# Kernel tuning notes

Hardware: AMD Instinct MI355X
Metric: run time of the kernel (lower is better)

## Reference

```python
import jax, jax.numpy as jnp
import numpy as np

IN_FEATURES = 64
WIDTH = 64
GRID_POINTS = 64   # num control points / basis functions
DEGREE = 3
BATCH = 32768
LN_EPS = 1e-5


def make_knots():
    # clamped knot vector on [0, 1]: length = GRID_POINTS + DEGREE + 1
    knot_count = GRID_POINTS + DEGREE + 1
    knots = np.zeros(knot_count, dtype=np.float32)
    knots[-(DEGREE + 1):] = 1.0
    interior = knot_count - 2 * (DEGREE + 1)
    if interior > 0:
        knots[DEGREE + 1: DEGREE + 1 + interior] = np.linspace(0.0, 1.0, interior + 2, dtype=np.float32)[1:-1]
    return jnp.asarray(knots)


def bspline_basis(x, knots):
    # x: [B, F] in (0,1); vectorized Cox-de Boor across batch and features
    xx = x[..., None]                      # [B, F, 1]
    left, right = knots[:-1], knots[1:]
    b = ((xx >= left) & (xx < right)).astype(x.dtype)      # [B, F, n_basis]
    last = ((x >= left[-1]) & (x <= right[-1])).astype(x.dtype)
    b = jnp.concatenate([b[..., :-1], last[..., None]], axis=-1)
    n_basis = knots.shape[0] - 1
    for d in range(1, DEGREE + 1):
        upper = n_basis - d
        i = np.arange(upper)
        k_i, k_id = knots[i], knots[i + d]
        k_i1, k_id1 = knots[i + 1], knots[i + d + 1]
        den1, den2 = k_id - k_i, k_id1 - k_i1
        w1 = jnp.where(den1 > 0, (xx - k_i) / jnp.where(den1 > 0, den1, 1.0), 0.0)
        w2 = jnp.where(den2 > 0, (k_id1 - xx) / jnp.where(den2 > 0, den2, 1.0), 0.0)
        b = w1 * b[..., :upper] + w2 * b[..., 1:upper + 1]
    return b  # [B, F, GRID_POINTS]


def setup_inputs() -> dict:
    key = jax.random.key(0)
    ks = jax.random.split(key, 6)
    coeff_init = float(np.sqrt(2.0 / (GRID_POINTS * IN_FEATURES)))
    return {
        "inputs": jax.random.normal(ks[0], (BATCH, IN_FEATURES), dtype=jnp.float32),
        "input_shift": 0.1 * jax.random.normal(ks[1], (IN_FEATURES,), dtype=jnp.float32),
        "input_log_scale": 0.1 * jax.random.normal(ks[2], (IN_FEATURES,), dtype=jnp.float32),
        "spline_coeffs": coeff_init * jax.random.normal(ks[3], (IN_FEATURES, GRID_POINTS, WIDTH), dtype=jnp.float32),
        "skip_W": jax.random.normal(ks[4], (WIDTH, IN_FEATURES), dtype=jnp.float32) / np.sqrt(IN_FEATURES),
        "skip_b": 0.01 * jax.random.normal(ks[5], (WIDTH,), dtype=jnp.float32),
        "bias": jnp.zeros((WIDTH,), dtype=jnp.float32),
        "ln_gamma": jnp.ones((WIDTH,), dtype=jnp.float32),
        "ln_beta": jnp.zeros((WIDTH,), dtype=jnp.float32),
        "knots": make_knots(),
    }


def reference(inputs, input_shift, input_log_scale, spline_coeffs, skip_W, skip_b, bias, ln_gamma, ln_beta, knots):
    scale = jax.nn.softplus(input_log_scale) + 0.001
    normalised = jax.nn.sigmoid((inputs - input_shift) * scale)     # [B, F]
    basis = bspline_basis(normalised, knots)                        # [B, F, G]
    spline_mix = jnp.einsum('bfg,fgw->bw', basis, spline_coeffs)    # [B, W]
    skip = inputs @ skip_W.T + skip_b
    c = spline_mix + skip + bias
    mean = jnp.mean(c, axis=-1, keepdims=True)
    var = jnp.mean((c - mean) ** 2, axis=-1, keepdims=True)
    y = (c - mean) / jnp.sqrt(var + LN_EPS) * ln_gamma + ln_beta
    return jax.nn.gelu(y, approximate=False)
```

## Files before the change

### kernel.cpp

```cpp
#include <hip/hip_runtime.h>
#include <math.h>


#define NTHREADS 512
#define ROWSB 32
#define SLABF 16384

typedef short bf16x8 __attribute__((ext_vector_type(8)));
typedef float f32x4  __attribute__((ext_vector_type(4)));

#if __has_builtin(__builtin_amdgcn_sdot4)
#define SDOT4(a, b, c) __builtin_amdgcn_sdot4((int)(a), (int)(b), (c), false)
#else
__device__ __forceinline__ int sdot4_sw(unsigned a, unsigned b, int c) {
    return c + (int)(signed char)(a) * (int)(signed char)(b)
             + (int)(signed char)(a >> 8)  * (int)(signed char)(b >> 8)
             + (int)(signed char)(a >> 16) * (int)(signed char)(b >> 16)
             + (int)(signed char)(a >> 24) * (int)(signed char)(b >> 24);
}
#define SDOT4(a, b, c) sdot4_sw((a), (b), (c))
#endif

__device__ __forceinline__ unsigned int f2bf1(float f) {
    unsigned int u = __float_as_uint(f);
    return (u + 0x7fffu + ((u >> 16) & 1u)) >> 16;
}
__device__ __forceinline__ unsigned int q8(float v) {
    const float s = fminf(fmaxf(v * 512.f, -127.f), 127.f);
    return (unsigned int)((int)rintf(s)) & 255u;
}

__global__ __launch_bounds__(256) void kan_prep(
    const float* __restrict__ coeff_g,
    unsigned char* __restrict__ ws8)
{
    const int idx = blockIdx.x * 256 + threadIdx.x;
    const int f = idx / 3904;
    const int rem = idx - f * 3904;
    const int g0 = rem >> 6, w = rem & 63;
    const float* src = coeff_g + ((size_t)f << 12) + (g0 << 6) + w;
    const unsigned int d = q8(src[0])
                         | (q8(src[64])  << 8)
                         | (q8(src[128]) << 16)
                         | (q8(src[192]) << 24);
    *(unsigned int*)(ws8 + ((size_t)f << 14) + (g0 << 8) + (w << 2)) = d;
}

#define DOT4Q(WP, AV) do { \
    doti[0] = SDOT4((WP), (AV).x, doti[0]); \
    doti[1] = SDOT4((WP), (AV).y, doti[1]); \
    doti[2] = SDOT4((WP), (AV).z, doti[2]); \
    doti[3] = SDOT4((WP), (AV).w, doti[3]); } while (0)

template<bool PRE>
__global__ __launch_bounds__(NTHREADS, 6) void kan_fused(
    const float* __restrict__ x_g,
    const float* __restrict__ shift_g,
    const float* __restrict__ lsc_g,
    const float* __restrict__ coeff_g,
    const float* __restrict__ skipW_g,
    const float* __restrict__ skipb_g,
    const float* __restrict__ bias_g,
    const float* __restrict__ gamma_g,
    const float* __restrict__ beta_g,
    const float* __restrict__ knots_g,
    const unsigned char* __restrict__ ws8,
    float* __restrict__ out_g)
{
    __shared__ float  xin[64][ROWSB];
    __shared__ unsigned short xb[32 * 64];
    __shared__ unsigned short wst[64 * 64];
    __shared__ float  skps[32][64];
    __shared__ uint2  wtabd[2][32][20];
    __shared__ float  knot_s[68];
    __shared__ float  scale_s[64];
    __shared__ float  shift_s[64];

    const int t = threadIdx.x;
    const int row0 = blockIdx.x * ROWSB;

    auto basis_group = [&](int gb) {
        const int fc_ = t >> 5, r_ = t & 31;
        const int feat = (gb << 4) + fc_;
        const float xs = (xin[feat][r_] - shift_s[feat]) * scale_s[feat];
        const float xq = 1.f / (1.f + __expf(-xs));
        int m = (int)floorf(xq * 61.f);
        m = m < 0 ? 0 : (m > 60 ? 60 : m);
        const float u = fmaf(xq, 61.f, -(float)m);
        float N0, N1, N2, N3;
        if (__builtin_expect(m >= 2 && m <= 58, 1)) {
            const float omu = 1.f - u;
            const float u2 = u * u, u3 = u2 * u;
            N0 = omu * omu * omu * (1.f / 6.f);
            N3 = u3 * (1.f / 6.f);
            N1 = 0.5f * u3 - u2 + (2.f / 3.f);
            N2 = 1.f - N0 - N1 - N3;
        } else {
            const int i = m + 3;
            float left[4], right[4], N[4];
            N[0] = 1.f;
            #pragma unroll
            for (int j = 1; j <= 3; ++j) {
                left[j]  = xq - knot_s[i + 1 - j];
                right[j] = knot_s[i + j] - xq;
                float saved = 0.f;
                #pragma unroll
                for (int rr = 0; rr < j; ++rr) {
                    const float temp = N[rr] * __builtin_amdgcn_rcpf(right[rr + 1] + left[j - rr]);
                    N[rr] = saved + right[rr + 1] * temp;
                    saved = left[j - rr] * temp;
                }
                N[j] = saved;
            }
            N0 = N[0]; N1 = N[1]; N2 = N[2]; N3 = N[3];
        }
        const unsigned int q0 = (unsigned int)(int)(fmaxf(N0, 0.f) * 126.f + 0.5f);
        const unsigned int q1 = (unsigned int)(int)(fmaxf(N1, 0.f) * 126.f + 0.5f);
        const unsigned int q2 = (unsigned int)(int)(fmaxf(N2, 0.f) * 126.f + 0.5f);
        const unsigned int q3 = (unsigned int)(int)(fmaxf(N3, 0.f) * 126.f + 0.5f);
        wtabd[gb & 1][r_][fc_] = make_uint2(q0 | (q1 << 8) | (q2 << 16) | (q3 << 24),
                                            (unsigned int)(m << 8));
    };

    {
        const int r = t >> 4, f0 = (t & 15) << 2;
        const float4 a = *((const float4*)(x_g + (size_t)(row0 + r) * 64 + f0));
        xin[f0 + 0][r] = a.x; xin[f0 + 1][r] = a.y;
        xin[f0 + 2][r] = a.z; xin[f0 + 3][r] = a.w;
        uint2 p;
        p.x = f2bf1(a.x) | (f2bf1(a.y) << 16);
        p.y = f2bf1(a.z) | (f2bf1(a.w) << 16);
        const int byte = r * 128 + ((((t & 15) << 3)) ^ ((r & 7) << 4));
        *(uint2*)((char*)xb + byte) = p;
    }
    {
        const int w = t >> 3, f0 = (t & 7) << 3;
        const float4* src = (const float4*)(skipW_g + (size_t)w * 64 + f0);
        const float4 a0 = src[0], a1 = src[1];
        uint4 p;
        p.x = f2bf1(a0.x) | (f2bf1(a0.y) << 16);
        p.y = f2bf1(a0.z) | (f2bf1(a0.w) << 16);
        p.z = f2bf1(a1.x) | (f2bf1(a1.y) << 16);
        p.w = f2bf1(a1.z) | (f2bf1(a1.w) << 16);
        const int byte = w * 128 + ((((t & 7) << 4)) ^ ((w & 7) << 4));
        *(uint4*)((char*)wst + byte) = p;
    }
    if (t < 64) {
        scale_s[t] = log1pf(__expf(lsc_g[t])) + 0.001f;
        shift_s[t] = shift_g[t];
    }
    if (t < 68) knot_s[t] = knots_g[t];
    __syncthreads();

    const int lane = t & 63;
    const int wave = t >> 6;

    {
        const int mtile = wave >> 2;
        const int ntile = wave & 3;
        const int arow = mtile * 16 + (lane & 15);
        const int bcol = ntile * 16 + (lane & 15);
        const int koff = (lane >> 4) << 4;
        f32x4 acc = {0.f, 0.f, 0.f, 0.f};
        #pragma unroll
        for (int kb = 0; kb < 2; ++kb) {
            const int kbyte = (kb << 6) + koff;
            const bf16x8 af = *(const bf16x8*)((const char*)xb
                                + arow * 128 + (kbyte ^ ((arow & 7) << 4)));
            const bf16x8 bfr = *(const bf16x8*)((const char*)wst
                                + bcol * 128 + (kbyte ^ ((bcol & 7) << 4)));
            acc = __builtin_amdgcn_mfma_f32_16x16x32_bf16(af, bfr, acc, 0, 0, 0);
        }
        #pragma unroll
        for (int rr = 0; rr < 4; ++rr)
            skps[mtile * 16 + ((lane >> 4) << 2) + rr][bcol] = acc[rr];
    }

    const int wc   = lane & 15;
    const int rsub = lane >> 4;
    const int row  = (wave << 2) + rsub;
    const int w4   = wc << 2;
    const int wcb  = wc << 4;

    int doti[4] = {0, 0, 0, 0};
    float facc[4] = {0.f, 0.f, 0.f, 0.f};

    basis_group(0);
    __syncthreads();

    for (int g = 0; g < 4; ++g) {
        const uint2* wrow = &wtabd[g & 1][row][0];
        if (PRE) {
            const unsigned char* const gbase = ws8 + ((size_t)g << 18);
            const uint4 wpa = *(const uint4*)(wrow + 0);
            const uint4 wpb = *(const uint4*)(wrow + 2);
            const uint4 wpc = *(const uint4*)(wrow + 4);
            const uint4 wpd = *(const uint4*)(wrow + 6);
            const uint4 A0 = *(const uint4*)(gbase + (0 << 14) + (wpa.y | wcb));
            const uint4 A1 = *(const uint4*)(gbase + (1 << 14) + (wpa.w | wcb));
            const uint4 A2 = *(const uint4*)(gbase + (2 << 14) + (wpb.y | wcb));
            const uint4 A3 = *(const uint4*)(gbase + (3 << 14) + (wpb.w | wcb));
            const uint4 A4 = *(const uint4*)(gbase + (4 << 14) + (wpc.y | wcb));
            const uint4 A5 = *(const uint4*)(gbase + (5 << 14) + (wpc.w | wcb));
            const uint4 A6 = *(const uint4*)(gbase + (6 << 14) + (wpd.y | wcb));
            const uint4 A7 = *(const uint4*)(gbase + (7 << 14) + (wpd.w | wcb));
            if (g < 3) basis_group(g + 1);
            DOT4Q(wpa.x, A0); DOT4Q(wpa.z, A1);
            DOT4Q(wpb.x, A2); DOT4Q(wpb.z, A3);
            DOT4Q(wpc.x, A4); DOT4Q(wpc.z, A5);
            DOT4Q(wpd.x, A6); DOT4Q(wpd.z, A7);
            const uint4 wpe = *(const uint4*)(wrow + 8);
            const uint4 wpf = *(const uint4*)(wrow + 10);
            const uint4 wpg = *(const uint4*)(wrow + 12);
            const uint4 wph = *(const uint4*)(wrow + 14);
            const uint4 B0 = *(const uint4*)(gbase + (8 << 14)  + (wpe.y | wcb));
            const uint4 B1 = *(const uint4*)(gbase + (9 << 14)  + (wpe.w | wcb));
            const uint4 B2 = *(const uint4*)(gbase + (10 << 14) + (wpf.y | wcb));
            const uint4 B3 = *(const uint4*)(gbase + (11 << 14) + (wpf.w | wcb));
            const uint4 B4 = *(const uint4*)(gbase + (12 << 14) + (wpg.y | wcb));
            const uint4 B5 = *(const uint4*)(gbase + (13 << 14) + (wpg.w | wcb));
            const uint4 B6 = *(const uint4*)(gbase + (14 << 14) + (wph.y | wcb));
            const uint4 B7 = *(const uint4*)(gbase + (15 << 14) + (wph.w | wcb));
            DOT4Q(wpe.x, B0); DOT4Q(wpe.z, B1);
            DOT4Q(wpf.x, B2); DOT4Q(wpf.z, B3);
            DOT4Q(wpg.x, B4); DOT4Q(wpg.z, B5);
            DOT4Q(wph.x, B6); DOT4Q(wph.z, B7);
        } else {
            if (g < 3) basis_group(g + 1);
            #pragma unroll 2
            for (int fc = 0; fc < 16; ++fc) {
                const int f = (g << 4) + fc;
                const uint2 wv = wrow[fc];
                const float* cb = coeff_g + ((size_t)f << 12) + (wv.y >> 2) + w4;
                const float4 c0 = *((const float4*)cb);
                const float4 c1 = *((const float4*)(cb + 64));
                const float4 c2 = *((const float4*)(cb + 128));
                const float4 c3 = *((const float4*)(cb + 192));
                const float q0 = (float)(wv.x & 255u);
                const float q1 = (float)((wv.x >> 8) & 255u);
                const float q2 = (float)((wv.x >> 16) & 255u);
                const float q3 = (float)((wv.x >> 24) & 255u);
                facc[0] += q0 * c0.x + q1 * c1.x + q2 * c2.x + q3 * c3.x;
                facc[1] += q0 * c0.y + q1 * c1.y + q2 * c2.y + q3 * c3.y;
                facc[2] += q0 * c0.z + q1 * c1.z + q2 * c2.z + q3 * c3.z;
                facc[3] += q0 * c0.w + q1 * c1.w + q2 * c2.w + q3 * c3.w;
            }
        }
        __syncthreads();
    }

    const float4 sk = *((const float4*)(&skps[row][w4]));
    const float4 sb = *((const float4*)(skipb_g + w4));
    const float4 bi = *((const float4*)(bias_g + w4));
    const float4 ga = *((const float4*)(gamma_g + w4));
    const float4 be = *((const float4*)(beta_g + w4));
    const float add_[4] = {sk.x + sb.x + bi.x, sk.y + sb.y + bi.y,
                           sk.z + sb.z + bi.z, sk.w + sb.w + bi.w};
    const float gam[4] = {ga.x, ga.y, ga.z, ga.w};
    const float bet[4] = {be.x, be.y, be.z, be.w};
    const float cs = PRE ? (1.f / (512.f * 126.f)) : (1.f / 126.f);

    float c[4];
    #pragma unroll
    for (int k = 0; k < 4; ++k) {
        const float sp = PRE ? (float)doti[k] * cs : facc[k] * cs;
        c[k] = sp + add_[k];
    }
    float s = c[0] + c[1] + c[2] + c[3];
    s += __shfl_xor(s, 1); s += __shfl_xor(s, 2);
    s += __shfl_xor(s, 4); s += __shfl_xor(s, 8);
    const float mean = s * 0.015625f;
    float v = 0.f;
    #pragma unroll
    for (int k = 0; k < 4; ++k) { const float d = c[k] - mean; v += d * d; }
    v += __shfl_xor(v, 1); v += __shfl_xor(v, 2);
    v += __shfl_xor(v, 4); v += __shfl_xor(v, 8);
    const float inv = rsqrtf(v * 0.015625f + 1e-5f);
    float o[4];
    #pragma unroll
    for (int k = 0; k < 4; ++k) {
        const float y = (c[k] - mean) * inv * gam[k] + bet[k];
        o[k] = 0.5f * y * (1.f + erff(y * 0.70710678118f));
    }
    *((float4*)(out_g + (size_t)(row0 + row) * 64 + w4)) =
        make_float4(o[0], o[1], o[2], o[3]);
}

extern "C" void kernel_launch(void* const* d_in, const int* in_sizes, int n_in,
                              void* d_out, int out_size, void* d_ws, size_t ws_size,
                              hipStream_t stream) {
    (void)in_sizes; (void)n_in; (void)out_size;
    const bool pre = (ws_size >= (size_t)(64 * SLABF));
    if (pre) {
        kan_prep<<<976, 256, 0, stream>>>((const float*)d_in[3], (unsigned char*)d_ws);
        kan_fused<true><<<1024, NTHREADS, 0, stream>>>(
            (const float*)d_in[0], (const float*)d_in[1], (const float*)d_in[2],
            (const float*)d_in[3], (const float*)d_in[4], (const float*)d_in[5],
            (const float*)d_in[6], (const float*)d_in[7], (const float*)d_in[8],
            (const float*)d_in[9], (const unsigned char*)d_ws, (float*)d_out);
    } else {
        kan_fused<false><<<1024, NTHREADS, 0, stream>>>(
            (const float*)d_in[0], (const float*)d_in[1], (const float*)d_in[2],
            (const float*)d_in[3], (const float*)d_in[4], (const float*)d_in[5],
            (const float*)d_in[6], (const float*)d_in[7], (const float*)d_in[8],
            (const float*)d_in[9], (const unsigned char*)d_ws, (float*)d_out);
    }
}
```

Before: 35.41 us.

## Compute all basis weights upfront and run a single sync-free gather loop

Replaces the four-stage double-buffered basis/gather pipeline with one pass in which each thread computes basis weights for four features of a row. It writes them into a padded per-row table that aliases the shared-memory area already used by the skip-GEMM operands. The main loop then walks all 64 features with no per-group barriers. Launch bounds rise to 8 blocks per CU, and the aliasing shrinks LDS use to make room. The trade is the loss of overlap between basis computation and gather loads, and tighter register limits.

New measurement: 32.65 us. -7.8%, faster.

```diff
diff --git a/kernel.cpp b/kernel.cpp
--- a/kernel.cpp
+++ b/kernel.cpp
@@ -5,6 +5,7 @@
 #define NTHREADS 512
 #define ROWSB 32
 #define SLABF 16384
+#define WTROW 544
 
 typedef short bf16x8 __attribute__((ext_vector_type(8)));
 typedef float f32x4  __attribute__((ext_vector_type(4)));
@@ -53,7 +54,7 @@
     doti[3] = SDOT4((WP), (AV).w, doti[3]); } while (0)
 
 template<bool PRE>
-__global__ __launch_bounds__(NTHREADS, 6) void kan_fused(
+__global__ __launch_bounds__(NTHREADS, 8) void kan_fused(
     const float* __restrict__ x_g,
     const float* __restrict__ shift_g,
     const float* __restrict__ lsc_g,
@@ -67,60 +68,17 @@
     const unsigned char* __restrict__ ws8,
     float* __restrict__ out_g)
 {
-    __shared__ float  xin[64][ROWSB];
-    __shared__ unsigned short xb[32 * 64];
-    __shared__ unsigned short wst[64 * 64];
-    __shared__ float  skps[32][64];
-    __shared__ uint2  wtabd[2][32][20];
-    __shared__ float  knot_s[68];
-    __shared__ float  scale_s[64];
-    __shared__ float  shift_s[64];
+    __shared__ float xin[64][ROWSB];
+    __shared__ char  uA[32 * WTROW] __attribute__((aligned(16)));
+    __shared__ float skps[32][64];
+    __shared__ float knot_s[68];
+    __shared__ float scale_s[64];
+    __shared__ float shift_s[64];
+    unsigned short* const xb  = (unsigned short*)uA;
+    unsigned short* const wst = (unsigned short*)(uA + 4096);
 
     const int t = threadIdx.x;
     const int row0 = blockIdx.x * ROWSB;
-
-    auto basis_group = [&](int gb) {
-        const int fc_ = t >> 5, r_ = t & 31;
-        const int feat = (gb << 4) + fc_;
-        const float xs = (xin[feat][r_] - shift_s[feat]) * scale_s[feat];
-        const float xq = 1.f / (1.f + __expf(-xs));
-        int m = (int)floorf(xq * 61.f);
-        m = m < 0 ? 0 : (m > 60 ? 60 : m);
-        const float u = fmaf(xq, 61.f, -(float)m);
-        float N0, N1, N2, N3;
-        if (__builtin_expect(m >= 2 && m <= 58, 1)) {
-            const float omu = 1.f - u;
-            const float u2 = u * u, u3 = u2 * u;
-            N0 = omu * omu * omu * (1.f / 6.f);
-            N3 = u3 * (1.f / 6.f);
-            N1 = 0.5f * u3 - u2 + (2.f / 3.f);
-            N2 = 1.f - N0 - N1 - N3;
-        } else {
-            const int i = m + 3;
-            float left[4], right[4], N[4];
-            N[0] = 1.f;
-            #pragma unroll
-            for (int j = 1; j <= 3; ++j) {
-                left[j]  = xq - knot_s[i + 1 - j];
-                right[j] = knot_s[i + j] - xq;
-                float saved = 0.f;
-                #pragma unroll
-                for (int rr = 0; rr < j; ++rr) {
-                    const float temp = N[rr] * __builtin_amdgcn_rcpf(right[rr + 1] + left[j - rr]);
-                    N[rr] = saved + right[rr + 1] * temp;
-                    saved = left[j - rr] * temp;
-                }
-                N[j] = saved;
-            }
-            N0 = N[0]; N1 = N[1]; N2 = N[2]; N3 = N[3];
-        }
-        const unsigned int q0 = (unsigned int)(int)(fmaxf(N0, 0.f) * 126.f + 0.5f);
-        const unsigned int q1 = (unsigned int)(int)(fmaxf(N1, 0.f) * 126.f + 0.5f);
-        const unsigned int q2 = (unsigned int)(int)(fmaxf(N2, 0.f) * 126.f + 0.5f);
-        const unsigned int q3 = (unsigned int)(int)(fmaxf(N3, 0.f) * 126.f + 0.5f);
-        wtabd[gb & 1][r_][fc_] = make_uint2(q0 | (q1 << 8) | (q2 << 16) | (q3 << 24),
-                                            (unsigned int)(m << 8));
-    };
 
     {
         const int r = t >> 4, f0 = (t & 15) << 2;
@@ -175,6 +133,58 @@
         for (int rr = 0; rr < 4; ++rr)
             skps[mtile * 16 + ((lane >> 4) << 2) + rr][bcol] = acc[rr];
     }
+    __syncthreads();
+
+    {
+        const int r_ = t & 31, fc4 = t >> 5;
+        uint2 ent[4];
+        #pragma unroll
+        for (int j = 0; j < 4; ++j) {
+            const int feat = (fc4 << 2) + j;
+            const float xs = (xin[feat][r_] - shift_s[feat]) * scale_s[feat];
+            const float xq = 1.f / (1.f + __expf(-xs));
+            int m = (int)floorf(xq * 61.f);
+            m = m < 0 ? 0 : (m > 60 ? 60 : m);
+            const float u = fmaf(xq, 61.f, -(float)m);
+            float N0, N1, N2, N3;
+            if (__builtin_expect(m >= 2 && m <= 58, 1)) {
+                const float omu = 1.f - u;
+                const float u2 = u * u, u3 = u2 * u;
+                N0 = omu * omu * omu * (1.f / 6.f);
+                N3 = u3 * (1.f / 6.f);
+                N1 = 0.5f * u3 - u2 + (2.f / 3.f);
+                N2 = 1.f - N0 - N1 - N3;
+            } else {
+                const int i = m + 3;
+                float left[4], right[4], N[4];
+                N[0] = 1.f;
+                #pragma unroll
+                for (int jj = 1; jj <= 3; ++jj) {
+                    left[jj]  = xq - knot_s[i + 1 - jj];
+                    right[jj] = knot_s[i + jj] - xq;
+                    float saved = 0.f;
+                    #pragma unroll
+                    for (int rr = 0; rr < jj; ++rr) {
+                        const float temp = N[rr] * __builtin_amdgcn_rcpf(right[rr + 1] + left[jj - rr]);
+                        N[rr] = saved + right[rr + 1] * temp;
+                        saved = left[jj - rr] * temp;
+                    }
+                    N[jj] = saved;
+                }
+                N0 = N[0]; N1 = N[1]; N2 = N[2]; N3 = N[3];
+            }
+            const unsigned int q0 = (unsigned int)(int)(fmaxf(N0, 0.f) * 126.f + 0.5f);
+            const unsigned int q1 = (unsigned int)(int)(fmaxf(N1, 0.f) * 126.f + 0.5f);
+            const unsigned int q2 = (unsigned int)(int)(fmaxf(N2, 0.f) * 126.f + 0.5f);
+            const unsigned int q3 = (unsigned int)(int)(fmaxf(N3, 0.f) * 126.f + 0.5f);
+            ent[j] = make_uint2(q0 | (q1 << 8) | (q2 << 16) | (q3 << 24),
+                                (unsigned int)(m << 8));
+        }
+        uint4* dst = (uint4*)(uA + r_ * WTROW + (fc4 << 5));
+        dst[0] = make_uint4(ent[0].x, ent[0].y, ent[1].x, ent[1].y);
+        dst[1] = make_uint4(ent[2].x, ent[2].y, ent[3].x, ent[3].y);
+    }
+    __syncthreads();
 
     const int wc   = lane & 15;
     const int rsub = lane >> 4;
@@ -184,69 +194,48 @@
 
     int doti[4] = {0, 0, 0, 0};
     float facc[4] = {0.f, 0.f, 0.f, 0.f};
-
-    basis_group(0);
-    __syncthreads();
-
-    for (int g = 0; g < 4; ++g) {
-        const uint2* wrow = &wtabd[g & 1][row][0];
-        if (PRE) {
-            const unsigned char* const gbase = ws8 + ((size_t)g << 18);
-            const uint4 wpa = *(const uint4*)(wrow + 0);
-            const uint4 wpb = *(const uint4*)(wrow + 2);
-            const uint4 wpc = *(const uint4*)(wrow + 4);
-            const uint4 wpd = *(const uint4*)(wrow + 6);
-            const uint4 A0 = *(const uint4*)(gbase + (0 << 14) + (wpa.y | wcb));
-            const uint4 A1 = *(const uint4*)(gbase + (1 << 14) + (wpa.w | wcb));
-            const uint4 A2 = *(const uint4*)(gbase + (2 << 14) + (wpb.y | wcb));
-            const uint4 A3 = *(const uint4*)(gbase + (3 << 14) + (wpb.w | wcb));
-            const uint4 A4 = *(const uint4*)(gbase + (4 << 14) + (wpc.y | wcb));
-            const uint4 A5 = *(const uint4*)(gbase + (5 << 14) + (wpc.w | wcb));
-            const uint4 A6 = *(const uint4*)(gbase + (6 << 14) + (wpd.y | wcb));
-            const uint4 A7 = *(const uint4*)(gbase + (7 << 14) + (wpd.w | wcb));
-            if (g < 3) basis_group(g + 1);
+    const char* const wrowp = uA + row * WTROW;
+
+    if (PRE) {
+        const unsigned char* const gb = ws8 + wcb;
+        #pragma unroll
+        for (int f8 = 0; f8 < 8; ++f8) {
+            const char* const wp8 = wrowp + (f8 << 6);
+            const uint4 wpa = *(const uint4*)(wp8 + 0);
+            const uint4 wpb = *(const uint4*)(wp8 + 16);
+            const uint4 A0 = *(const uint4*)(gb + (((f8 << 3) + 0) << 14) + wpa.y);
+            const uint4 A1 = *(const uint4*)(gb + (((f8 << 3) + 1) << 14) + wpa.w);
+            const uint4 A2 = *(const uint4*)(gb + (((f8 << 3) + 2) << 14) + wpb.y);
+            const uint4 A3 = *(const uint4*)(gb + (((f8 << 3) + 3) << 14) + wpb.w);
             DOT4Q(wpa.x, A0); DOT4Q(wpa.z, A1);
             DOT4Q(wpb.x, A2); DOT4Q(wpb.z, A3);
-            DOT4Q(wpc.x, A4); DOT4Q(wpc.z, A5);
-            DOT4Q(wpd.x, A6); DOT4Q(wpd.z, A7);
-            const uint4 wpe = *(const uint4*)(wrow + 8);
-            const uint4 wpf = *(const uint4*)(wrow + 10);
-            const uint4 wpg = *(const uint4*)(wrow + 12);
-            const uint4 wph = *(const uint4*)(wrow + 14);
-            const uint4 B0 = *(const uint4*)(gbase + (8 << 14)  + (wpe.y | wcb));
-            const uint4 B1 = *(const uint4*)(gbase + (9 << 14)  + (wpe.w | wcb));
-            const uint4 B2 = *(const uint4*)(gbase + (10 << 14) + (wpf.y | wcb));
-            const uint4 B3 = *(const uint4*)(gbase + (11 << 14) + (wpf.w | wcb));
-            const uint4 B4 = *(const uint4*)(gbase + (12 << 14) + (wpg.y | wcb));
-            const uint4 B5 = *(const uint4*)(gbase + (13 << 14) + (wpg.w | wcb));
-            const uint4 B6 = *(const uint4*)(gbase + (14 << 14) + (wph.y | wcb));
-            const uint4 B7 = *(const uint4*)(gbase + (15 << 14) + (wph.w | wcb));
-            DOT4Q(wpe.x, B0); DOT4Q(wpe.z, B1);
-            DOT4Q(wpf.x, B2); DOT4Q(wpf.z, B3);
-            DOT4Q(wpg.x, B4); DOT4Q(wpg.z, B5);
-            DOT4Q(wph.x, B6); DOT4Q(wph.z, B7);
-        } else {
-            if (g < 3) basis_group(g + 1);
-            #pragma unroll 2
-            for (int fc = 0; fc < 16; ++fc) {
-                const int f = (g << 4) + fc;
-                const uint2 wv = wrow[fc];
-                const float* cb = coeff_g + ((size_t)f << 12) + (wv.y >> 2) + w4;
-                const float4 c0 = *((const float4*)cb);
-                const float4 c1 = *((const float4*)(cb + 64));
-                const float4 c2 = *((const float4*)(cb + 128));
-                const float4 c3 = *((const float4*)(cb + 192));
-                const float q0 = (float)(wv.x & 255u);
-                const float q1 = (float)((wv.x >> 8) & 255u);
-                const float q2 = (float)((wv.x >> 16) & 255u);
-                const float q3 = (float)((wv.x >> 24) & 255u);
-                facc[0] += q0 * c0.x + q1 * c1.x + q2 * c2.x + q3 * c3.x;
-                facc[1] += q0 * c0.y + q1 * c1.y + q2 * c2.y + q3 * c3.y;
-                facc[2] += q0 * c0.z + q1 * c1.z + q2 * c2.z + q3 * c3.z;
-                facc[3] += q0 * c0.w + q1 * c1.w + q2 * c2.w + q3 * c3.w;
-            }
-        }
-        __syncthreads();
+            const uint4 wpc = *(const uint4*)(wp8 + 32);
+            const uint4 wpd = *(const uint4*)(wp8 + 48);
+            const uint4 B0 = *(const uint4*)(gb + (((f8 << 3) + 4) << 14) + wpc.y);
+            const uint4 B1 = *(const uint4*)(gb + (((f8 << 3) + 5) << 14) + wpc.w);
+            const uint4 B2 = *(const uint4*)(gb + (((f8 << 3) + 6) << 14) + wpd.y);
+            const uint4 B3 = *(const uint4*)(gb + (((f8 << 3) + 7) << 14) + wpd.w);
+            DOT4Q(wpc.x, B0); DOT4Q(wpc.z, B1);
+            DOT4Q(wpd.x, B2); DOT4Q(wpd.z, B3);
+        }
+    } else {
+        #pragma unroll 4
+        for (int f = 0; f < 64; ++f) {
+            const uint2 wv = *(const uint2*)(wrowp + (f << 3));
+            const float* cb = coeff_g + ((size_t)f << 12) + (wv.y >> 2) + w4;
+            const float4 c0 = *((const float4*)cb);
+            const float4 c1 = *((const float4*)(cb + 64));
+            const float4 c2 = *((const float4*)(cb + 128));
+            const float4 c3 = *((const float4*)(cb + 192));
+            const float q0 = (float)(wv.x & 255u);
+            const float q1 = (float)((wv.x >> 8) & 255u);
+            const float q2 = (float)((wv.x >> 16) & 255u);
+            const float q3 = (float)((wv.x >> 24) & 255u);
+            facc[0] += q0 * c0.x + q1 * c1.x + q2 * c2.x + q3 * c3.x;
+            facc[1] += q0 * c0.y + q1 * c1.y + q2 * c2.y + q3 * c3.y;
+            facc[2] += q0 * c0.z + q1 * c1.z + q2 * c2.z + q3 * c3.z;
+            facc[3] += q0 * c0.w + q1 * c1.w + q2 * c2.w + q3 * c3.w;
+        }
     }
 
     const float4 sk = *((const float4*)(&skps[row][w4]));
```
